# Performance work log

Hardware: AMD Instinct MI355X
Metric: run time of the kernel (lower is better)

## Reference

```python
import jax, jax.numpy as jnp
import numpy as np

# Fixed problem geometry: B equal-sized graphs with contiguous node ids.
B, N, E, F_IN, H, C = 64, 1024, 655360, 128, 128, 10
K1 = int(np.ceil(0.8 * N))    # 820 nodes/graph kept by pool1
K2 = int(np.ceil(0.8 * K1))   # 656 nodes/graph kept by pool2


def setup_inputs() -> dict:
    key = jax.random.key(0)
    ks = jax.random.split(key, 12)
    x = jax.random.normal(ks[0], (B * N, F_IN), jnp.float32)
    # intra-graph random edges, E//B per graph
    e_per = E // B
    local = jax.random.randint(ks[1], (2, E), 0, N)
    off = jnp.repeat(jnp.arange(B, dtype=jnp.int32) * N, e_per)
    edge_index = (local + off[None, :]).astype(jnp.int32)
    batch = jnp.repeat(jnp.arange(B, dtype=jnp.int32), N)

    def lin(k, i, o):
        return jax.random.normal(k, (i, o), jnp.float32) / np.sqrt(i)

    return {
        "x": x, "edge_index": edge_index, "batch": batch,
        "Wl1": lin(ks[2], F_IN, H), "bl1": jnp.zeros((H,), jnp.float32), "Wr1": lin(ks[3], F_IN, H),
        "Wl2": lin(ks[4], H, H),    "bl2": jnp.zeros((H,), jnp.float32), "Wr2": lin(ks[5], H, H),
        "pw1": jax.random.normal(ks[6], (H,), jnp.float32) / np.sqrt(H),
        "pw2": jax.random.normal(ks[7], (H,), jnp.float32) / np.sqrt(H),
        "fW1": lin(ks[8], 2 * H, H), "fb1": jnp.zeros((H,), jnp.float32),
        "fW2": lin(ks[9], H, C),     "fb2": jnp.zeros((C,), jnp.float32),
    }


def _sage(x, src, dst, em, Wl, bl, Wr, n):
    # PyG SAGEConv (aggr='mean'): lin_l(mean_{j->i} x_j) + lin_r(x_i)
    msg = x[src] * em[:, None]                                   # [E, d]
    s = jax.ops.segment_sum(msg, dst, num_segments=n)            # [n, d]
    cnt = jax.ops.segment_sum(em, dst, num_segments=n)           # [n]
    mean = s / jnp.maximum(cnt, 1.0)[:, None]
    return mean @ Wl + bl + x @ Wr


def _topk_pool(x, src, dst, em, n_per, k, w):
    # PyG TopKPooling: score = tanh(x.w/||w||); keep top-k per graph; gate kept x by score.
    score = jnp.tanh(x @ w / jnp.linalg.norm(w))                 # [B*n_per]
    _, idx = jax.lax.top_k(score.reshape(B, n_per), k)           # [B, k]
    idx = jnp.sort(idx, axis=1)
    perm = (idx + (jnp.arange(B) * n_per)[:, None]).reshape(-1)  # global kept ids [B*k]
    nx = x[perm] * score[perm][:, None]
    # relabel edges; drop edges touching removed nodes via mask
    inv = jnp.full((B * n_per,), -1, jnp.int32).at[perm].set(jnp.arange(B * k, dtype=jnp.int32))
    ns, nd = inv[src], inv[dst]
    nm = em * (ns >= 0).astype(x.dtype) * (nd >= 0).astype(x.dtype)
    return nx, jnp.maximum(ns, 0), jnp.maximum(nd, 0), nm


def _readout(h, k):
    g = h.reshape(B, k, H)
    return jnp.concatenate([g.mean(axis=1), g.max(axis=1)], axis=1)  # [B, 2H]


def reference(x, edge_index, batch, Wl1, bl1, Wr1, Wl2, bl2, Wr2,
              pw1, pw2, fW1, fb1, fW2, fb2):
    src, dst = edge_index[0], edge_index[1]
    em = jnp.ones((E,), x.dtype)
    h = jax.nn.relu(_sage(x, src, dst, em, Wl1, bl1, Wr1, B * N))
    h, src, dst, em = _topk_pool(h, src, dst, em, N, K1, pw1)
    x1 = _readout(h, K1)
    h = jax.nn.relu(_sage(h, src, dst, em, Wl2, bl2, Wr2, B * K1))
    h, src, dst, em = _topk_pool(h, src, dst, em, K1, K2, pw2)
    x2 = _readout(h, K2)
    z = jax.nn.relu((x1 + x2) @ fW1 + fb1)
    # dropout is identity in eval mode
    return z @ fW2 + fb2
```

## Files before the change

kernel.cpp:

```cpp
#include <hip/hip_runtime.h>
#include <cstdint>
#include <cstddef>

namespace {

constexpr int kB    = 64;
constexpr int kN    = 1024;
constexpr int kE    = 655360;
constexpr int kEper = kE / kB;
constexpr int kH    = 128;
constexpr int kK1   = 820;
constexpr int kK2   = 656;
constexpr int kM1   = kB * kN;
constexpr int kM2   = kB * kK1;

typedef __attribute__((ext_vector_type(8))) short bf16x8;
typedef __attribute__((ext_vector_type(4))) float f32x4;

__device__ inline ushort f2bf(float f) {
  uint u = __float_as_uint(f);
  return (ushort)((u + 0x7fffu + ((u >> 16) & 1u)) >> 16);
}
__device__ inline float bf2f(ushort s) { return __uint_as_float(((uint)s) << 16); }

__device__ inline void cvt4(const float* f, uint* hh, uint* ll) {
#pragma unroll
  for (int i = 0; i < 2; ++i) {
    uint h;
    asm("v_cvt_pk_bf16_f32 %0, %1, %2" : "=v"(h) : "v"(f[2 * i]), "v"(f[2 * i + 1]));
    const float r0 = __uint_as_float(h << 16);
    const float r1 = __uint_as_float(h & 0xFFFF0000u);
    const float d0 = f[2 * i] - r0;
    const float d1 = f[2 * i + 1] - r1;
    uint l;
    asm("v_cvt_pk_bf16_f32 %0, %1, %2" : "=v"(l) : "v"(d0), "v"(d1));
    hh[i] = h; ll[i] = l;
  }
}

__device__ inline void llds16(const void* g, void* l) {
  __builtin_amdgcn_global_load_lds(
      (const __attribute__((address_space(1))) void*)g,
      (__attribute__((address_space(3))) void*)l, 16, 0, 0);
}

__device__ inline int block_scan_1024(int v, int* wsum ) {
  const int lane = threadIdx.x & 63;
  const int w    = threadIdx.x >> 6;
#pragma unroll
  for (int off = 1; off < 64; off <<= 1) {
    const int n = __shfl_up(v, off);
    if (lane >= off) v += n;
  }
  if (lane == 63) wsum[w] = v;
  __syncthreads();
  if (w == 0) {
    int s = (lane < 16) ? wsum[lane] : 0;
#pragma unroll
    for (int off = 1; off < 16; off <<= 1) {
      const int n = __shfl_up(s, off);
      if (lane >= off) s += n;
    }
    if (lane < 16) wsum[lane] = s;
  }
  __syncthreads();
  if (w > 0) v += wsum[w - 1];
  return v;
}

__device__ inline void radix_select(uint key, int K, int* hist, uint* bTp,
                                    int* bRemp, uint& T, int& rem_out) {
  const int tid = threadIdx.x;
  uint prefix = 0;
  int rem = K;
#pragma unroll
  for (int shift = 24; shift >= 0; shift -= 8) {
    if (tid < 256) hist[tid] = 0;
    __syncthreads();
    const uint mask = (shift == 24) ? 0u : (0xFFFFFFFFu << (shift + 8));
    if ((key & mask) == prefix)
      atomicAdd(&hist[(key >> shift) & 255], 1);
    __syncthreads();
    if (tid < 64) {
      const int h0 = hist[4 * tid + 0], h1 = hist[4 * tid + 1];
      const int h2 = hist[4 * tid + 2], h3 = hist[4 * tid + 3];
      const int loc = h0 + h1 + h2 + h3;
      int suf = loc;
#pragma unroll
      for (int d = 1; d < 64; d <<= 1) {
        const int o = __shfl_down(suf, d);
        if (tid + d < 64) suf += o;
      }
      const int above = suf - loc;
      int hs[5];
      hs[4] = above;
      hs[3] = above + h3;
      hs[2] = hs[3] + h2;
      hs[1] = hs[2] + h1;
      hs[0] = hs[1] + h0;
#pragma unroll
      for (int q = 0; q < 4; ++q) {
        if (hs[q] >= rem && hs[q + 1] < rem) {
          *bTp   = prefix | ((uint)(4 * tid + q) << shift);
          *bRemp = rem - hs[q + 1];
        }
      }
    }
    __syncthreads();
    prefix = *bTp;
    rem    = *bRemp;
    __syncthreads();
  }
  T = prefix;
  rem_out = rem;
}

__device__ inline uint score_key(float sc) {
  const uint bits = __float_as_uint(sc);
  return (bits & 0x80000000u) ? ~bits : (bits | 0x80000000u);
}

__global__ __launch_bounds__(1024)
void build_prep(const int* __restrict__ src, const int* __restrict__ dst,
                int* __restrict__ coff, int* __restrict__ ccur,
                int* __restrict__ ent,
                const float* __restrict__ Wl1, const float* __restrict__ Wr1,
                const float* __restrict__ Wl2, const float* __restrict__ Wr2,
                const float* __restrict__ pw1, const float* __restrict__ pw2,
                ushort* __restrict__ W1h, ushort* __restrict__ W1l,
                ushort* __restrict__ W2h, ushort* __restrict__ W2l,
                float* __restrict__ pwn1, float* __restrict__ pwn2) {
  const int b   = blockIdx.x;
  const int tid = threadIdx.x;
  if (b >= 128) {
    if (tid >= 256) return;
    const float* pw = (tid < 128) ? pw1 : pw2;
    float* o        = (tid < 128) ? pwn1 : pwn2;
    const int j = tid & 127;
    float sum = 0.0f;
    for (int k = 0; k < 128; ++k) { const float v = pw[k]; sum += v * v; }
    o[j] = pw[j] / sqrtf(sum);
    return;
  }
  if (b >= 64) {
    const int ob  = (b - 64) * 4 + (tid >> 8);
    const bool l2 = ob >= 128;
    const int idx = (ob & 127) * 256 + (tid & 255);
    const int n = idx >> 8, k = idx & 255;
    const float* Wl = l2 ? Wl2 : Wl1;
    const float* Wr = l2 ? Wr2 : Wr1;
    const float w = (k < 128) ? Wl[k * kH + n] : Wr[(k - 128) * kH + n];
    const ushort h = f2bf(w);
    (l2 ? W2h : W1h)[n * 256 + k] = h;
    (l2 ? W2l : W1l)[n * 256 + k] = f2bf(w - bf2f(h));
    return;
  }
  __shared__ int cnt[1024];
  __shared__ int wsum[16];
  const int g = b;
  const int ebase = g * kEper;
  cnt[tid] = 0;
  __syncthreads();
  for (int e = tid; e < kEper; e += 1024)
    atomicAdd(&cnt[dst[ebase + e] & (kN - 1)], 1);
  __syncthreads();
  const int dg   = cnt[tid];
  const int incl = block_scan_1024(dg, wsum);
  const int start = ebase + incl - dg;
  coff[g * kN + tid] = start;
  ccur[g * kN + tid] = start + dg;
  __syncthreads();
  cnt[tid] = start;
  __syncthreads();
  for (int e = tid; e < kEper; e += 1024) {
    const int d   = dst[ebase + e] & (kN - 1);
    const int pos = atomicAdd(&cnt[d], 1);
    ent[pos] = src[ebase + e] & (kN - 1);
  }
}

__global__ __launch_bounds__(1024, 8)
void gather1_lds(const float* __restrict__ feat, const int* __restrict__ ent,
                 const int* __restrict__ off, const int* __restrict__ cursor,
                 float* __restrict__ aggout) {
  __shared__ float cache[1024 * 16];
  const int xcd   = blockIdx.x & 7;
  const int local = blockIdx.x >> 3;
  const int graph = xcd * 8 + (local >> 3);
  const int chunk = local & 7;
  const int tid   = threadIdx.x;
  const int wid   = tid >> 6;
  const int gbase = graph << 10;

#pragma unroll
  for (int ps = 0; ps < 4; ++ps) {
    const int row = ps * 256 + (tid >> 2);
    const int q   = (tid & 3) * 4;
    llds16(feat + (size_t)(gbase + row) * kH + chunk * 16 + q,
           cache + ps * 4096 + wid * 256);
  }
  __syncthreads();

  const int grp = tid >> 2;
  const int q4  = (tid & 3) * 4;

  for (int it = 0; it < 4; ++it) {
    const int lnode = it * 256 + grp;
    const int node  = gbase + lnode;
    const int o0 = off[node];
    const int o1 = cursor[node];
    const int deg = o1 - o0;
    float4 acc = make_float4(0.f, 0.f, 0.f, 0.f);
    int pf[4];
#pragma unroll
    for (int i = 0; i < 4; ++i) pf[i] = (o0 + i < o1) ? ent[o0 + i] : 0;
    for (int eb = 0; eb < deg; eb += 4) {
      int nx[4];
#pragma unroll
      for (int i = 0; i < 4; ++i) {
        const int idx = o0 + eb + 4 + i;
        nx[i] = (idx < o1) ? ent[idx] : 0;
      }
#pragma unroll
      for (int i = 0; i < 4; ++i) {
        const float m = (eb + i < deg) ? 1.0f : 0.0f;
        const float4 v = *(const float4*)&cache[pf[i] * 16 + q4];
        acc.x = fmaf(v.x, m, acc.x);
        acc.y = fmaf(v.y, m, acc.y);
        acc.z = fmaf(v.z, m, acc.z);
        acc.w = fmaf(v.w, m, acc.w);
      }
#pragma unroll
      for (int i = 0; i < 4; ++i) pf[i] = nx[i];
    }
    const float r = 1.0f / fmaxf((float)deg, 1.0f);
    const f32x4 res = {acc.x * r, acc.y * r, acc.z * r, acc.w * r};
    __builtin_nontemporal_store(res, (f32x4*)(aggout + (size_t)node * kH + chunk * 16 + q4));
  }
}

__global__ __launch_bounds__(1024, 8)
void gather2_lds(const float* __restrict__ feat, const int* __restrict__ ent,
                 const int* __restrict__ off, const int* __restrict__ cursor,
                 const int* __restrict__ perm, const float* __restrict__ gsg,
                 float* __restrict__ aggout,
                 float* __restrict__ psumg, float* __restrict__ pmaxg) {
  __shared__ float cache[1024 * 16];
  __shared__ float gs[1024];
  __shared__ float rps[16][16], rpm[16][16];
  const int xcd   = blockIdx.x & 7;
  const int local = blockIdx.x >> 3;
  const int graph = xcd * 8 + (local >> 3);
  const int chunk = local & 7;
  const int tid   = threadIdx.x;
  const int wid   = tid >> 6;
  const int gbase = graph << 10;

#pragma unroll
  for (int ps = 0; ps < 4; ++ps) {
    const int row = ps * 256 + (tid >> 2);
    const int q   = (tid & 3) * 4;
    llds16(feat + (size_t)(gbase + row) * kH + chunk * 16 + q,
           cache + ps * 4096 + wid * 256);
  }
  gs[tid] = gsg[gbase + tid];
  __syncthreads();

  const int grp = tid >> 2;
  const int q4  = (tid & 3) * 4;

  for (int it = 0; it < 4; ++it) {
    const int lnode = it * 256 + grp;
    int o0 = 0, o1 = 0;
    if (lnode < kK1) {
      const int orig = perm[graph * kK1 + lnode];
      o0 = off[orig];
      o1 = cursor[orig];
    }
    const int deg = o1 - o0;
    float4 acc = make_float4(0.f, 0.f, 0.f, 0.f);
    int cnt = 0;
    int pf[4];
#pragma unroll
    for (int i = 0; i < 4; ++i) pf[i] = (o0 + i < o1) ? ent[o0 + i] : 0;
    for (int eb = 0; eb < deg; eb += 4) {
      int nx[4];
#pragma unroll
      for (int i = 0; i < 4; ++i) {
        const int idx = o0 + eb + 4 + i;
        nx[i] = (idx < o1) ? ent[idx] : 0;
      }
#pragma unroll
      for (int i = 0; i < 4; ++i) {
        const float raw  = gs[pf[i]];
        const bool  kept = (raw > 0.5f) && (eb + i < deg);
        const float s    = kept ? raw - 2.0f : 0.0f;
        cnt += kept ? 1 : 0;
        const float4 v = *(const float4*)&cache[pf[i] * 16 + q4];
        acc.x = fmaf(v.x, s, acc.x);
        acc.y = fmaf(v.y, s, acc.y);
        acc.z = fmaf(v.z, s, acc.z);
        acc.w = fmaf(v.w, s, acc.w);
      }
#pragma unroll
      for (int i = 0; i < 4; ++i) pf[i] = nx[i];
    }
    const float r = 1.0f / fmaxf((float)cnt, 1.0f);
    const f32x4 res = {acc.x * r, acc.y * r, acc.z * r, acc.w * r};
    if (lnode < kK1)
      __builtin_nontemporal_store(res,
          (f32x4*)(aggout + (size_t)(graph * kK1 + lnode) * kH + chunk * 16 + q4));
  }

  __syncthreads();
  const int rcol = tid & 15;
  const int rseg = tid >> 4;
  float rs = 0.0f, rm = -1e30f;
#pragma unroll
  for (int i = 0; i < 16; ++i) {
    const int row = rseg * 16 + i;
    const float raw = gs[row];
    if (raw > 0.5f) {
      const float v = cache[row * 16 + rcol] * (raw - 2.0f);
      rs += v;
      rm = fmaxf(rm, v);
    }
  }
  rs += __shfl_xor(rs, 16); rs += __shfl_xor(rs, 32);
  rm = fmaxf(rm, __shfl_xor(rm, 16)); rm = fmaxf(rm, __shfl_xor(rm, 32));
  if ((tid & 48) == 0) { rps[wid][rcol] = rs; rpm[wid][rcol] = rm; }
  __syncthreads();
  if (tid < 16) {
    float ts = 0.0f, tm = -1e30f;
#pragma unroll
    for (int w = 0; w < 16; ++w) { ts += rps[w][tid]; tm = fmaxf(tm, rpm[w][tid]); }
    psumg[graph * kH + chunk * 16 + tid] = ts;
    pmaxg[graph * kH + chunk * 16 + tid] = tm;
  }
}

__global__ __launch_bounds__(256)
void sage_gemm_mfma(const float* __restrict__ meanb, const float* __restrict__ xsrc,
                    const int* __restrict__ perm, const float* __restrict__ gsc,
                    const ushort* __restrict__ WTh, const ushort* __restrict__ WTl,
                    const float* __restrict__ bias, const float* __restrict__ pwn,
                    float* __restrict__ outp, float* __restrict__ scr) {
  __shared__ __align__(16) ushort aH[64][32];
  __shared__ __align__(16) ushort aL[64][32];
  __shared__ __align__(16) ushort wHs[128][32];
  __shared__ __align__(16) ushort wLs[128][32];
  __shared__ float sdot[64][2];
  const int tid  = threadIdx.x;
  const int wid  = tid >> 6;
  const int lane = tid & 63;
  const int quad = lane >> 4;
  const int l16  = lane & 15;
  const int rowbase = blockIdx.x * 64;
  const int wr = (wid >> 1) * 32;
  const int wc = (wid & 1) * 64;

  const int n0a = wid * 32;
  const int n0b = wid * 32 + 16;
  const int wrowa = (n0a + (lane >> 2)) * 256 + (lane & 3) * 8;
  const int wrowb = (n0b + (lane >> 2)) * 256 + (lane & 3) * 8;

  int srow1[2]; float scl1[2];
#pragma unroll
  for (int i = 0; i < 2; ++i) {
    const int grow = rowbase + ((tid + i * 256) >> 3);
    srow1[i] = grow; scl1[i] = 1.0f;
    if (perm) { srow1[i] = perm[grow]; scl1[i] = gsc[grow]; }
  }

  f32x4 acc[2][4];
#pragma unroll
  for (int a = 0; a < 2; ++a)
#pragma unroll
    for (int b = 0; b < 4; ++b) acc[a][b] = (f32x4){0.f, 0.f, 0.f, 0.f};

  for (int s = 0; s < 8; ++s) {
    const bool ismean = s < 4;
    const float* sp = ismean ? meanb : xsrc;
    const int kbase = s * 32;
    const int kloc  = ismean ? kbase : kbase - 128;
#pragma unroll
    for (int i = 0; i < 2; ++i) {
      const int p   = tid + i * 256;
      const int row = p >> 3;
      const int k4  = (p & 7) * 4;
      const int srow   = ismean ? (rowbase + row) : srow1[i];
      const float scale = ismean ? 1.0f : scl1[i];
      const float4 v = *(const float4*)(sp + (size_t)srow * kH + kloc + k4);
      float f[4] = {v.x * scale, v.y * scale, v.z * scale, v.w * scale};
      uint hh[2], ll[2];
      cvt4(f, hh, ll);
      *(uint2*)&aH[row][k4] = make_uint2(hh[0], hh[1]);
      *(uint2*)&aL[row][k4] = make_uint2(ll[0], ll[1]);
    }
    llds16(WTh + wrowa + kbase, &wHs[n0a][0]);
    llds16(WTh + wrowb + kbase, &wHs[n0b][0]);
    llds16(WTl + wrowa + kbase, &wLs[n0a][0]);
    llds16(WTl + wrowb + kbase, &wLs[n0b][0]);
    __syncthreads();
    bf16x8 afh[2], afl[2];
#pragma unroll
    for (int rt = 0; rt < 2; ++rt) {
      afh[rt] = *(const bf16x8*)&aH[wr + rt * 16 + l16][quad * 8];
      afl[rt] = *(const bf16x8*)&aL[wr + rt * 16 + l16][quad * 8];
    }
#pragma unroll
    for (int ct = 0; ct < 4; ++ct) {
      const bf16x8 bh = *(const bf16x8*)&wHs[wc + ct * 16 + l16][quad * 8];
      const bf16x8 bl = *(const bf16x8*)&wLs[wc + ct * 16 + l16][quad * 8];
#pragma unroll
      for (int rt = 0; rt < 2; ++rt) {
        acc[rt][ct] = __builtin_amdgcn_mfma_f32_16x16x32_bf16(afh[rt], bh, acc[rt][ct], 0, 0, 0);
        acc[rt][ct] = __builtin_amdgcn_mfma_f32_16x16x32_bf16(afh[rt], bl, acc[rt][ct], 0, 0, 0);
        acc[rt][ct] = __builtin_amdgcn_mfma_f32_16x16x32_bf16(afl[rt], bh, acc[rt][ct], 0, 0, 0);
      }
    }
    __syncthreads();
  }
  float bv[4], pwv[4];
#pragma unroll
  for (int ct = 0; ct < 4; ++ct) {
    const int col = wc + ct * 16 + l16;
    bv[ct]  = bias[col];
    pwv[ct] = pwn[col];
  }
  float dot[2][4];
#pragma unroll
  for (int rt = 0; rt < 2; ++rt)
#pragma unroll
    for (int reg = 0; reg < 4; ++reg) dot[rt][reg] = 0.0f;
#pragma unroll
  for (int ct = 0; ct < 4; ++ct) {
    const int col = wc + ct * 16 + l16;
#pragma unroll
    for (int rt = 0; rt < 2; ++rt) {
#pragma unroll
      for (int reg = 0; reg < 4; ++reg) {
        const int row = rowbase + wr + rt * 16 + quad * 4 + reg;
        const float o = fmaxf(acc[rt][ct][reg] + bv[ct], 0.0f);
        outp[(size_t)row * kH + col] = o;
        dot[rt][reg] += o * pwv[ct];
      }
    }
  }
#pragma unroll
  for (int rt = 0; rt < 2; ++rt) {
#pragma unroll
    for (int reg = 0; reg < 4; ++reg) {
      float d = dot[rt][reg];
      d += __shfl_xor(d, 1);
      d += __shfl_xor(d, 2);
      d += __shfl_xor(d, 4);
      d += __shfl_xor(d, 8);
      if (l16 == 0) sdot[wr + rt * 16 + quad * 4 + reg][wc >> 6] = d;
    }
  }
  __syncthreads();
  if (tid < 64) scr[rowbase + tid] = tanhf(sdot[tid][0] + sdot[tid][1]);
}

__global__ __launch_bounds__(1024)
void rank_compact(const float* __restrict__ scr, int n_per, int K,
                  int* __restrict__ perm, float* __restrict__ gsc,
                  float* __restrict__ gsg) {
  __shared__ int hist[256];
  __shared__ int wsum[16];
  __shared__ uint bT;
  __shared__ int bRem;
  const int g = blockIdx.x, tid = threadIdx.x;
  const float sc = (tid < n_per) ? scr[g * n_per + tid] : -3e30f;
  const uint key = score_key(sc);

  uint T; int rem;
  radix_select(key, K, hist, &bT, &bRem, T, rem);

  const int gt = (key > T) ? 1 : 0;
  const int eq = (key == T) ? 1 : 0;
  const int incl = block_scan_1024((gt << 11) | eq, wsum);
  const int excl = incl - ((gt << 11) | eq);
  const int gt_excl = excl >> 11;
  const int eq_excl = excl & 2047;
  const int keep = (tid < n_per) && (gt || (eq && eq_excl < rem));
  if (keep) {
    const int pos = gt_excl + min(eq_excl, rem);
    perm[g * K + pos] = g * n_per + tid;
    gsc[g * K + pos]  = sc;
  }
  if (gsg) gsg[g * kN + tid] = keep ? sc + 2.0f : 0.0f;
}

__global__ __launch_bounds__(1024)
void final_fused(const float* __restrict__ scr, const float* __restrict__ h2,
                 const float* __restrict__ ps1, const float* __restrict__ pm1,
                 const float* __restrict__ fW1, const float* __restrict__ fb1,
                 const float* __restrict__ fW2, const float* __restrict__ fb2,
                 float* __restrict__ out) {
  __shared__ int hist[256];
  __shared__ int wsum[16];
  __shared__ uint bT;
  __shared__ int bRem;
  __shared__ float ls[1024];
  __shared__ float ss[8][128], sm[8][128];
  __shared__ float xx[256];
  __shared__ float z[128];
  const int g = blockIdx.x, tid = threadIdx.x;
  const int n_per = kK1, K = kK2;

  const float sc = (tid < n_per) ? scr[g * n_per + tid] : -3e30f;
  const uint key = score_key(sc);
  uint T; int rem;
  radix_select(key, K, hist, &bT, &bRem, T, rem);
  const int gt = (key > T) ? 1 : 0;
  const int eq = (key == T) ? 1 : 0;
  const int eq_incl = block_scan_1024(eq, wsum);
  const int eq_excl = eq_incl - eq;
  const int keep = (tid < n_per) && (gt || (eq && eq_excl < rem));
  ls[tid] = keep ? sc + 2.0f : 0.0f;
  __syncthreads();

  const int part = tid >> 7;
  const int j    = tid & 127;
  const float* h2g = h2 + (size_t)g * kK1 * kH + j;
  float sum = 0.0f, mx = -1e30f;
  for (int i = part; i < n_per; i += 32) {
    float v[4], s[4];
#pragma unroll
    for (int u = 0; u < 4; ++u) {
      const int ii = i + u * 8;
      const bool ok = ii < n_per;
      s[u] = ok ? ls[ii] : 0.0f;
      v[u] = ok ? h2g[(size_t)ii * kH] : 0.0f;
    }
#pragma unroll
    for (int u = 0; u < 4; ++u) {
      const float val = v[u] * (s[u] - 2.0f);
      if (s[u] > 0.5f) { sum += val; mx = fmaxf(mx, val); }
    }
  }
  ss[part][j] = sum;
  sm[part][j] = mx;
  __syncthreads();

  if (tid < 128) {
    float s2 = 0.0f, m2 = -1e30f;
#pragma unroll
    for (int p = 0; p < 8; ++p) { s2 += ss[p][tid]; m2 = fmaxf(m2, sm[p][tid]); }
    const float s1 = ps1[(size_t)g * 128 + tid];
    const float m1 = pm1[(size_t)g * 128 + tid];
    xx[tid]       = s1 / (float)kK1 + s2 / (float)K;
    xx[tid + 128] = m1 + m2;
  }
  __syncthreads();
  if (tid < 128) {
    float a = fb1[tid];
    for (int k = 0; k < 256; ++k) a += xx[k] * fW1[k * 128 + tid];
    z[tid] = fmaxf(a, 0.0f);
  }
  __syncthreads();
  if (tid < 10) {
    float o = fb2[tid];
    for (int k = 0; k < 128; ++k) o += z[k] * fW2[k * 10 + tid];
    out[g * 10 + tid] = o;
  }
}

}

extern "C" void kernel_launch(void* const* d_in, const int* in_sizes, int n_in,
                              void* d_out, int out_size, void* d_ws, size_t ws_size,
                              hipStream_t stream) {
  const float* x   = (const float*)d_in[0];
  const int*   ei  = (const int*)d_in[1];
  const float* Wl1 = (const float*)d_in[3];
  const float* bl1 = (const float*)d_in[4];
  const float* Wr1 = (const float*)d_in[5];
  const float* Wl2 = (const float*)d_in[6];
  const float* bl2 = (const float*)d_in[7];
  const float* Wr2 = (const float*)d_in[8];
  const float* pw1 = (const float*)d_in[9];
  const float* pw2 = (const float*)d_in[10];
  const float* fW1 = (const float*)d_in[11];
  const float* fb1 = (const float*)d_in[12];
  const float* fW2 = (const float*)d_in[13];
  const float* fb2 = (const float*)d_in[14];
  const int* src = ei;
  const int* dst = ei + kE;
  (void)in_sizes; (void)n_in; (void)out_size; (void)ws_size;

  char* wsb = (char*)d_ws;
  size_t off_b = 0;
  auto alloc = [&](size_t bytes) {
    void* p = wsb + off_b;
    off_b += (bytes + 255) & ~(size_t)255;
    return p;
  };
  float* bufA = (float*)alloc((size_t)kM1 * kH * 4);
  float* bufB = (float*)alloc((size_t)kM1 * kH * 4);
  float* bufC = (float*)alloc((size_t)kM2 * kH * 4);
  int*   coff = (int*)alloc((size_t)kM1 * 4);
  int*   ccur = (int*)alloc((size_t)kM1 * 4);
  int*   ent  = (int*)alloc((size_t)kE * 4);
  float* scr  = (float*)alloc((size_t)kM1 * 4);
  float* gsg  = (float*)alloc((size_t)kM1 * 4);
  int*   perm1= (int*)alloc((size_t)kM2 * 4);
  float* gsc1 = (float*)alloc((size_t)kM2 * 4);
  float* psum1= (float*)alloc((size_t)kB * 128 * 4);
  float* pmax1= (float*)alloc((size_t)kB * 128 * 4);
  ushort* wt1h = (ushort*)alloc((size_t)128 * 256 * 2);
  ushort* wt1l = (ushort*)alloc((size_t)128 * 256 * 2);
  ushort* wt2h = (ushort*)alloc((size_t)128 * 256 * 2);
  ushort* wt2l = (ushort*)alloc((size_t)128 * 256 * 2);
  float* pwn1 = (float*)alloc(128 * 4);
  float* pwn2 = (float*)alloc(128 * 4);

  build_prep<<<129, 1024, 0, stream>>>(src, dst, coff, ccur, ent,
                                       Wl1, Wr1, Wl2, Wr2, pw1, pw2,
                                       wt1h, wt1l, wt2h, wt2l, pwn1, pwn2);

  gather1_lds<<<kB * 8, 1024, 0, stream>>>(x, ent, coff, ccur, bufA);
  sage_gemm_mfma<<<kM1 / 64, 256, 0, stream>>>(bufA, x, nullptr, nullptr,
                                               wt1h, wt1l, bl1, pwn1, bufB, scr);
  rank_compact<<<kB, 1024, 0, stream>>>(scr, kN, kK1, perm1, gsc1, gsg);

  gather2_lds<<<kB * 8, 1024, 0, stream>>>(bufB, ent, coff, ccur, perm1, gsg,
                                           bufA, psum1, pmax1);
  sage_gemm_mfma<<<kM2 / 64, 256, 0, stream>>>(bufA, bufB, perm1, gsc1,
                                               wt2h, wt2l, bl2, pwn2, bufC, scr);

  final_fused<<<kB, 1024, 0, stream>>>(scr, bufC, psum1, pmax1,
                                       fW1, fb1, fW2, fb2, (float*)d_out);
}
```

Measured before the change: 238.4 us.

## Sort nodes by degree so gather warps process similar-degree nodes together

Builds a per-graph counting sort of nodes by in-degree in build_prep and a degree-sorted ordering of kept nodes in rank_compact. The gather kernels then assign node slots through these orderings, so lanes in one wavefront handle nodes with similar degree. The goal is less divergence and fewer idle lanes in the variable-length neighbour loops. It costs an extra histogram and scan pass in two kernels, an extra indirection load, and writes to output rows that are no longer contiguous.

```diff
diff --git a/kernel.cpp b/kernel.cpp
--- a/kernel.cpp
+++ b/kernel.cpp
@@ -123,7 +123,7 @@
 __global__ __launch_bounds__(1024)
 void build_prep(const int* __restrict__ src, const int* __restrict__ dst,
                 int* __restrict__ coff, int* __restrict__ ccur,
-                int* __restrict__ ent,
+                int* __restrict__ ent, int* __restrict__ nodeord,
                 const float* __restrict__ Wl1, const float* __restrict__ Wr1,
                 const float* __restrict__ Wl2, const float* __restrict__ Wr2,
                 const float* __restrict__ pw1, const float* __restrict__ pw2,
@@ -177,12 +177,24 @@
     const int pos = atomicAdd(&cnt[d], 1);
     ent[pos] = src[ebase + e] & (kN - 1);
   }
+  __syncthreads();
+  const int degc = min(dg, 1023);
+  cnt[tid] = 0;
+  __syncthreads();
+  atomicAdd(&cnt[degc], 1);
+  __syncthreads();
+  const int hcnt  = cnt[tid];
+  const int hincl = block_scan_1024(hcnt, wsum);
+  cnt[tid] = hincl - hcnt;
+  __syncthreads();
+  const int spos = atomicAdd(&cnt[degc], 1);
+  nodeord[g * kN + spos] = tid;
 }
 
 __global__ __launch_bounds__(1024, 8)
 void gather1_lds(const float* __restrict__ feat, const int* __restrict__ ent,
                  const int* __restrict__ off, const int* __restrict__ cursor,
-                 float* __restrict__ aggout) {
+                 const int* __restrict__ nodeord, float* __restrict__ aggout) {
   __shared__ float cache[1024 * 16];
   const int xcd   = blockIdx.x & 7;
   const int local = blockIdx.x >> 3;
@@ -205,7 +217,8 @@
   const int q4  = (tid & 3) * 4;
 
   for (int it = 0; it < 4; ++it) {
-    const int lnode = it * 256 + grp;
+    const int slot  = it * 256 + grp;
+    const int lnode = nodeord[gbase + slot];
     const int node  = gbase + lnode;
     const int o0 = off[node];
     const int o1 = cursor[node];
@@ -242,7 +255,7 @@
 __global__ __launch_bounds__(1024, 8)
 void gather2_lds(const float* __restrict__ feat, const int* __restrict__ ent,
                  const int* __restrict__ off, const int* __restrict__ cursor,
-                 const int* __restrict__ perm, const float* __restrict__ gsg,
+                 const int* __restrict__ kperm, const float* __restrict__ gsg,
                  float* __restrict__ aggout,
                  float* __restrict__ psumg, float* __restrict__ pmaxg) {
   __shared__ float cache[1024 * 16];
@@ -270,10 +283,12 @@
   const int q4  = (tid & 3) * 4;
 
   for (int it = 0; it < 4; ++it) {
-    const int lnode = it * 256 + grp;
-    int o0 = 0, o1 = 0;
-    if (lnode < kK1) {
-      const int orig = perm[graph * kK1 + lnode];
+    const int slot = it * 256 + grp;
+    int o0 = 0, o1 = 0, lnode = 0;
+    if (slot < kK1) {
+      const int e = kperm[graph * kK1 + slot];
+      lnode = e & 1023;
+      const int orig = gbase + (e >> 10);
       o0 = off[orig];
       o1 = cursor[orig];
     }
@@ -307,7 +322,7 @@
     }
     const float r = 1.0f / fmaxf((float)cnt, 1.0f);
     const f32x4 res = {acc.x * r, acc.y * r, acc.z * r, acc.w * r};
-    if (lnode < kK1)
+    if (slot < kK1)
       __builtin_nontemporal_store(res,
           (f32x4*)(aggout + (size_t)(graph * kK1 + lnode) * kH + chunk * 16 + q4));
   }
@@ -466,8 +481,10 @@
 __global__ __launch_bounds__(1024)
 void rank_compact(const float* __restrict__ scr, int n_per, int K,
                   int* __restrict__ perm, float* __restrict__ gsc,
-                  float* __restrict__ gsg) {
-  __shared__ int hist[256];
+                  float* __restrict__ gsg,
+                  const int* __restrict__ coff, const int* __restrict__ ccur,
+                  int* __restrict__ kperm) {
+  __shared__ int hist[1024];
   __shared__ int wsum[16];
   __shared__ uint bT;
   __shared__ int bRem;
@@ -485,12 +502,30 @@
   const int gt_excl = excl >> 11;
   const int eq_excl = excl & 2047;
   const int keep = (tid < n_per) && (gt || (eq && eq_excl < rem));
+  const int pos  = gt_excl + min(eq_excl, rem);
   if (keep) {
-    const int pos = gt_excl + min(eq_excl, rem);
     perm[g * K + pos] = g * n_per + tid;
     gsc[g * K + pos]  = sc;
   }
   if (gsg) gsg[g * kN + tid] = keep ? sc + 2.0f : 0.0f;
+
+  if (kperm) {
+    const int deg  = ccur[g * kN + tid] - coff[g * kN + tid];
+    const int degc = min(deg, 1023);
+    __syncthreads();
+    hist[tid] = 0;
+    __syncthreads();
+    if (keep) atomicAdd(&hist[degc], 1);
+    __syncthreads();
+    const int hcnt  = hist[tid];
+    const int hincl = block_scan_1024(hcnt, wsum);
+    hist[tid] = hincl - hcnt;
+    __syncthreads();
+    if (keep) {
+      const int spos = atomicAdd(&hist[degc], 1);
+      kperm[g * kK1 + spos] = (tid << 10) | pos;
+    }
+  }
 }
 
 __global__ __launch_bounds__(1024)
@@ -604,10 +639,12 @@
   int*   coff = (int*)alloc((size_t)kM1 * 4);
   int*   ccur = (int*)alloc((size_t)kM1 * 4);
   int*   ent  = (int*)alloc((size_t)kE * 4);
+  int*   nodeord = (int*)alloc((size_t)kM1 * 4);
   float* scr  = (float*)alloc((size_t)kM1 * 4);
   float* gsg  = (float*)alloc((size_t)kM1 * 4);
   int*   perm1= (int*)alloc((size_t)kM2 * 4);
   float* gsc1 = (float*)alloc((size_t)kM2 * 4);
+  int*   kperm1 = (int*)alloc((size_t)kM2 * 4);
   float* psum1= (float*)alloc((size_t)kB * 128 * 4);
   float* pmax1= (float*)alloc((size_t)kB * 128 * 4);
   ushort* wt1h = (ushort*)alloc((size_t)128 * 256 * 2);
@@ -617,16 +654,17 @@
   float* pwn1 = (float*)alloc(128 * 4);
   float* pwn2 = (float*)alloc(128 * 4);
 
-  build_prep<<<129, 1024, 0, stream>>>(src, dst, coff, ccur, ent,
+  build_prep<<<129, 1024, 0, stream>>>(src, dst, coff, ccur, ent, nodeord,
                                        Wl1, Wr1, Wl2, Wr2, pw1, pw2,
                                        wt1h, wt1l, wt2h, wt2l, pwn1, pwn2);
 
-  gather1_lds<<<kB * 8, 1024, 0, stream>>>(x, ent, coff, ccur, bufA);
+  gather1_lds<<<kB * 8, 1024, 0, stream>>>(x, ent, coff, ccur, nodeord, bufA);
   sage_gemm_mfma<<<kM1 / 64, 256, 0, stream>>>(bufA, x, nullptr, nullptr,
                                                wt1h, wt1l, bl1, pwn1, bufB, scr);
-  rank_compact<<<kB, 1024, 0, stream>>>(scr, kN, kK1, perm1, gsc1, gsg);
-
-  gather2_lds<<<kB * 8, 1024, 0, stream>>>(bufB, ent, coff, ccur, perm1, gsg,
+  rank_compact<<<kB, 1024, 0, stream>>>(scr, kN, kK1, perm1, gsc1, gsg,
+                                        coff, ccur, kperm1);
+
+  gather2_lds<<<kB * 8, 1024, 0, stream>>>(bufB, ent, coff, ccur, kperm1, gsg,
                                            bufA, psum1, pmax1);
   sage_gemm_mfma<<<kM2 / 64, 256, 0, stream>>>(bufA, bufB, perm1, gsc1,
                                                wt2h, wt2l, bl2, pwn2, bufC, scr);
```

Result: no change. 242.7 us (+1.8%).
